# Performance work log

Hardware: AMD Instinct MI355X
Metric: run time of the kernel (lower is better)

Reference implementation:

```python
import jax, jax.numpy as jnp
import numpy as np

NUM_EXPERTS = 64


def setup_inputs() -> dict:
    key = jax.random.key(0)
    k1, k2 = jax.random.split(key)
    x = jax.random.normal(k1, (8192, 4096), dtype=jnp.float32)
    W = jax.random.normal(k2, (NUM_EXPERTS, 4096), dtype=jnp.float32) * 0.02
    return {"x": x, "W": W}


def reference(x, W):
    # gate: logits = x @ W^T  -> [T, E]
    logits = jnp.einsum('th,eh->te', x, W)
    scores = jax.nn.softmax(logits, axis=-1)
    # top_k == 1 path: max with keepdim (torch scores.max(dim=-1, keepdim=True))
    expert_weights = jnp.max(scores, axis=-1, keepdims=True)      # [T, 1]
    expert_indices = jnp.argmax(scores, axis=-1, keepdims=True)   # [T, 1] int
    # routing_counts = bincount(expert_indices.squeeze(1), minlength=E)
    routing_counts = jnp.bincount(expert_indices[:, 0], length=NUM_EXPERTS)
    return (expert_weights, expert_indices, scores, routing_counts)
```

## Files before the change

### kernel.cpp

```cpp
#include <hip/hip_runtime.h>
#include <stdint.h>

#define T_TOKENS 8192
#define K_DIM    4096
#define NEXP     64
#define TB       128
#define KC       64

typedef short bf16x8 __attribute__((ext_vector_type(8)));
typedef float f32x4  __attribute__((ext_vector_type(4)));

__device__ __forceinline__ uint32_t f2bf(float v) {
    uint32_t u = __builtin_bit_cast(uint32_t, v);
    return (u + 0x7fffu + ((u >> 16) & 1u)) >> 16;
}
__device__ __forceinline__ float bf2f(uint32_t b) {
    return __builtin_bit_cast(float, b << 16);
}
struct S3 { short h, l, q; };
__device__ __forceinline__ S3 cvt1(float v) {
    uint32_t hb = f2bf(v); float r  = v - bf2f(hb);
    uint32_t lb = f2bf(r); float r2 = r - bf2f(lb);
    uint32_t qb = f2bf(r2);
    S3 o; o.h = (short)hb; o.l = (short)lb; o.q = (short)qb; return o;
}
__device__ __forceinline__ void cvt8(const float4 a0, const float4 a1,
                                     bf16x8& xh, bf16x8& xl, bf16x8& xq) {
    const float av[8] = {a0.x, a0.y, a0.z, a0.w, a1.x, a1.y, a1.z, a1.w};
#pragma unroll
    for (int j = 0; j < 8; ++j) {
        S3 o = cvt1(av[j]);
        xh[j] = o.h; xl[j] = o.l; xq[j] = o.q;
    }
}

__global__ void wpack(const float* __restrict__ W, float4* __restrict__ Wf,
                      float* __restrict__ out_counts) {
    const int l     = threadIdx.x;
    const int kstep = blockIdx.x;
    const int etile = blockIdx.y;
    if (kstep == 0 && etile == 0)
        out_counts[l] = 0.f;
    const int e = etile * 16 + (l & 15);
    const int k = kstep * 32 + (l >> 4) * 8;
    const float* src = W + (size_t)e * K_DIM + k;
    bf16x8 h, l1, l2;
#pragma unroll
    for (int j = 0; j < 8; ++j) {
        S3 o = cvt1(src[j]);
        h[j] = o.h; l1[j] = o.l; l2[j] = o.q;
    }
    const size_t base = ((size_t)(kstep * 4 + etile) * 3) * 64 + l;
    Wf[base]       = __builtin_bit_cast(float4, h);
    Wf[base + 64]  = __builtin_bit_cast(float4, l1);
    Wf[base + 128] = __builtin_bit_cast(float4, l2);
}

__global__ __launch_bounds__(512, 4) void gemm_mfma(
    const float*  __restrict__ x,
    const float4* __restrict__ Wf,
    float* __restrict__ P,
    int KS)
{
    __shared__ float4 bbuf[2][1536];

    const int tid  = threadIdx.x;
    const int l    = tid & 63;
    const int wv   = __builtin_amdgcn_readfirstlane(tid >> 6);
    const int t0   = blockIdx.x * TB;
    const int slice = blockIdx.y;
    const int k0   = slice * KS;
    const int nchunk = KS / KC;

    const float4* x4 = (const float4*)x;
    const int arow = wv * 16 + (l & 15);
    const size_t xg = (size_t)(t0 + arow) * (K_DIM / 4) + (size_t)(k0 >> 2) + ((l >> 4) * 2);

    const size_t bg0 = ((size_t)(k0 >> 5)) * 768;

    f32x4 acc[4];
#pragma unroll
    for (int et = 0; et < 4; ++et) acc[et] = (f32x4){0.f, 0.f, 0.f, 0.f};

#pragma unroll
    for (int q = 0; q < 3; ++q)
        __builtin_amdgcn_global_load_lds(
            (const __attribute__((address_space(1))) void*)(Wf + bg0 + (wv * 3 + q) * 64 + l),
            (__attribute__((address_space(3))) void*)&bbuf[0][(wv * 3 + q) * 64],
            16, 0, 0);
    float4 xa0 = x4[xg + 0], xa1 = x4[xg + 1];
    float4 xa2 = x4[xg + 8], xa3 = x4[xg + 9];
    asm volatile("s_waitcnt vmcnt(0)" ::: "memory");
    __syncthreads();

    for (int c = 0; c < nchunk; ++c) {
        const int b  = c & 1;
        const int nb = b ^ 1;

        float4 xn0 = xa0, xn1 = xa1, xn2 = xa2, xn3 = xa3;
        if (c + 1 < nchunk) {
            const size_t bo = bg0 + (size_t)(c + 1) * 1536;
#pragma unroll
            for (int q = 0; q < 3; ++q)
                __builtin_amdgcn_global_load_lds(
                    (const __attribute__((address_space(1))) void*)(Wf + bo + (wv * 3 + q) * 64 + l),
                    (__attribute__((address_space(3))) void*)&bbuf[nb][(wv * 3 + q) * 64],
                    16, 0, 0);
            const size_t xo = xg + (size_t)(c + 1) * 16;
            xn0 = x4[xo + 0]; xn1 = x4[xo + 1];
            xn2 = x4[xo + 8]; xn3 = x4[xo + 9];
        }

        bf16x8 xh0, xl0, xq0, xh1, xl1, xq1;
        cvt8(xa0, xa1, xh0, xl0, xq0);
        cvt8(xa2, xa3, xh1, xl1, xq1);

#pragma unroll
        for (int et = 0; et < 4; ++et) {
            {
                const float4* bp = &bbuf[b][et * 192 + l];
                bf16x8 wh = __builtin_bit_cast(bf16x8, bp[0]);
                bf16x8 wl = __builtin_bit_cast(bf16x8, bp[64]);
                bf16x8 wq = __builtin_bit_cast(bf16x8, bp[128]);
                acc[et] = __builtin_amdgcn_mfma_f32_16x16x32_bf16(xh0, wh, acc[et], 0, 0, 0);
                acc[et] = __builtin_amdgcn_mfma_f32_16x16x32_bf16(xh0, wl, acc[et], 0, 0, 0);
                acc[et] = __builtin_amdgcn_mfma_f32_16x16x32_bf16(xh0, wq, acc[et], 0, 0, 0);
                acc[et] = __builtin_amdgcn_mfma_f32_16x16x32_bf16(xl0, wh, acc[et], 0, 0, 0);
                acc[et] = __builtin_amdgcn_mfma_f32_16x16x32_bf16(xl0, wl, acc[et], 0, 0, 0);
                acc[et] = __builtin_amdgcn_mfma_f32_16x16x32_bf16(xq0, wh, acc[et], 0, 0, 0);
            }
            {
                const float4* bp = &bbuf[b][768 + et * 192 + l];
                bf16x8 wh = __builtin_bit_cast(bf16x8, bp[0]);
                bf16x8 wl = __builtin_bit_cast(bf16x8, bp[64]);
                bf16x8 wq = __builtin_bit_cast(bf16x8, bp[128]);
                acc[et] = __builtin_amdgcn_mfma_f32_16x16x32_bf16(xh1, wh, acc[et], 0, 0, 0);
                acc[et] = __builtin_amdgcn_mfma_f32_16x16x32_bf16(xh1, wl, acc[et], 0, 0, 0);
                acc[et] = __builtin_amdgcn_mfma_f32_16x16x32_bf16(xh1, wq, acc[et], 0, 0, 0);
                acc[et] = __builtin_amdgcn_mfma_f32_16x16x32_bf16(xl1, wh, acc[et], 0, 0, 0);
                acc[et] = __builtin_amdgcn_mfma_f32_16x16x32_bf16(xl1, wl, acc[et], 0, 0, 0);
                acc[et] = __builtin_amdgcn_mfma_f32_16x16x32_bf16(xq1, wh, acc[et], 0, 0, 0);
            }
        }

        asm volatile("s_waitcnt vmcnt(0)" ::: "memory");
        __syncthreads();
        xa0 = xn0; xa1 = xn1; xa2 = xn2; xa3 = xn3;
    }

    float* Pp = P + (size_t)slice * T_TOKENS * NEXP;
#pragma unroll
    for (int et = 0; et < 4; ++et) {
#pragma unroll
        for (int i = 0; i < 4; ++i) {
            int t = t0 + wv * 16 + (l >> 4) * 4 + i;
            Pp[(size_t)t * NEXP + et * 16 + (l & 15)] = acc[et][i];
        }
    }
}

template <int S>
__global__ __launch_bounds__(256) void router_finish_t(
    const float* __restrict__ P, float* __restrict__ out)
{
    const int lane = threadIdx.x & 63;
    const int wv   = threadIdx.x >> 6;
    const int t    = blockIdx.x * 4 + wv;

    float lg = 0.f;
#pragma unroll
    for (int s = 0; s < S; ++s)
        lg += P[((size_t)s * T_TOKENS + t) * NEXP + lane];

    float* out_w = out;
    float* out_i = out + T_TOKENS;
    float* out_s = out + 2 * T_TOKENS;
    float* out_c = out + 2 * T_TOKENS + (size_t)T_TOKENS * NEXP;

    float m = lg;
#pragma unroll
    for (int off = 32; off > 0; off >>= 1)
        m = fmaxf(m, __shfl_xor(m, off));
    float p = expf(lg - m);
    float s = p;
#pragma unroll
    for (int off = 32; off > 0; off >>= 1)
        s += __shfl_xor(s, off);
    float sc = p / s;

    float bv = sc; int bi = lane;
#pragma unroll
    for (int off = 32; off > 0; off >>= 1) {
        float ov = __shfl_xor(bv, off);
        int   oi = __shfl_xor(bi, off);
        if (ov > bv || (ov == bv && oi < bi)) { bv = ov; bi = oi; }
    }
    out_s[(size_t)t * NEXP + lane] = sc;
    if (lane == 0) {
        out_w[t] = bv;
        out_i[t] = (float)bi;
        atomicAdd(&out_c[bi], 1.0f);
    }
}

extern "C" void kernel_launch(void* const* d_in, const int* in_sizes, int n_in,
                              void* d_out, int out_size, void* d_ws, size_t ws_size,
                              hipStream_t stream)
{
    const float* x = (const float*)d_in[0];
    const float* W = (const float*)d_in[1];
    float* out = (float*)d_out;
    float* out_s = out + 2 * T_TOKENS;
    float* out_c = out + 2 * T_TOKENS + (size_t)T_TOKENS * NEXP;

    const size_t wf_bytes  = (size_t)128 * 4 * 3 * 64 * 16;
    const size_t per_slice = (size_t)T_TOKENS * NEXP * sizeof(float);

    int S = 8;
    while (S > 1 && wf_bytes + (size_t)S * per_slice > ws_size) S >>= 1;
    float4* Wf = (float4*)d_ws;
    float* Pbuf;
    if (wf_bytes + per_slice <= ws_size) {
        Pbuf = (float*)((char*)d_ws + wf_bytes);
    } else {
        S = 1;
        Pbuf = out_s;
    }

    wpack<<<dim3(128, 4), 64, 0, stream>>>(W, Wf, out_c);
    gemm_mfma<<<dim3(T_TOKENS / TB, S), 512, 0, stream>>>(x, Wf, Pbuf, K_DIM / S);
    switch (S) {
        case 8: router_finish_t<8><<<T_TOKENS / 4, 256, 0, stream>>>(Pbuf, out); break;
        case 4: router_finish_t<4><<<T_TOKENS / 4, 256, 0, stream>>>(Pbuf, out); break;
        case 2: router_finish_t<2><<<T_TOKENS / 4, 256, 0, stream>>>(Pbuf, out); break;
        default: router_finish_t<1><<<T_TOKENS / 4, 256, 0, stream>>>(Pbuf, out); break;
    }
}
```

Baseline: 93.63 us.

## Replace LDS-staged GEMM with register-pipelined 2x2 wave tiling and direct weight loads

```diff
diff --git a/kernel.cpp b/kernel.cpp
--- a/kernel.cpp
+++ b/kernel.cpp
@@ -5,7 +5,6 @@
 #define K_DIM    4096
 #define NEXP     64
 #define TB       128
-#define KC       64
 
 typedef short bf16x8 __attribute__((ext_vector_type(8)));
 typedef float f32x4  __attribute__((ext_vector_type(4)));
@@ -56,105 +55,90 @@
     Wf[base + 128] = __builtin_bit_cast(float4, l2);
 }
 
-__global__ __launch_bounds__(512, 4) void gemm_mfma(
+template <int NCH>
+__global__ __launch_bounds__(512, 2) void gemm_mfma(
     const float*  __restrict__ x,
     const float4* __restrict__ Wf,
-    float* __restrict__ P,
-    int KS)
+    float* __restrict__ P)
 {
-    __shared__ float4 bbuf[2][1536];
-
     const int tid  = threadIdx.x;
     const int l    = tid & 63;
     const int wv   = __builtin_amdgcn_readfirstlane(tid >> 6);
-    const int t0   = blockIdx.x * TB;
-    const int slice = blockIdx.y;
-    const int k0   = slice * KS;
-    const int nchunk = KS / KC;
+    const int rg   = wv >> 1;
+    const int cg   = wv & 1;
+    const int slice = blockIdx.x;
+    const int t0    = blockIdx.y * TB;
+    const int k0    = slice * (NCH * 32);
 
     const float4* x4 = (const float4*)x;
-    const int arow = wv * 16 + (l & 15);
-    const size_t xg = (size_t)(t0 + arow) * (K_DIM / 4) + (size_t)(k0 >> 2) + ((l >> 4) * 2);
-
-    const size_t bg0 = ((size_t)(k0 >> 5)) * 768;
-
-    f32x4 acc[4];
-#pragma unroll
-    for (int et = 0; et < 4; ++et) acc[et] = (f32x4){0.f, 0.f, 0.f, 0.f};
-
-#pragma unroll
-    for (int q = 0; q < 3; ++q)
-        __builtin_amdgcn_global_load_lds(
-            (const __attribute__((address_space(1))) void*)(Wf + bg0 + (wv * 3 + q) * 64 + l),
-            (__attribute__((address_space(3))) void*)&bbuf[0][(wv * 3 + q) * 64],
-            16, 0, 0);
-    float4 xa0 = x4[xg + 0], xa1 = x4[xg + 1];
-    float4 xa2 = x4[xg + 8], xa3 = x4[xg + 9];
-    asm volatile("s_waitcnt vmcnt(0)" ::: "memory");
-    __syncthreads();
-
-    for (int c = 0; c < nchunk; ++c) {
-        const int b  = c & 1;
-        const int nb = b ^ 1;
-
-        float4 xn0 = xa0, xn1 = xa1, xn2 = xa2, xn3 = xa3;
-        if (c + 1 < nchunk) {
-            const size_t bo = bg0 + (size_t)(c + 1) * 1536;
-#pragma unroll
-            for (int q = 0; q < 3; ++q)
-                __builtin_amdgcn_global_load_lds(
-                    (const __attribute__((address_space(1))) void*)(Wf + bo + (wv * 3 + q) * 64 + l),
-                    (__attribute__((address_space(3))) void*)&bbuf[nb][(wv * 3 + q) * 64],
-                    16, 0, 0);
-            const size_t xo = xg + (size_t)(c + 1) * 16;
-            xn0 = x4[xo + 0]; xn1 = x4[xo + 1];
-            xn2 = x4[xo + 8]; xn3 = x4[xo + 9];
+    const size_t xr0 = (size_t)(t0 + rg * 32 + (l & 15)) * (K_DIM / 4)
+                     + (size_t)(k0 >> 2) + ((l >> 4) * 2);
+    const size_t xr1 = xr0 + (size_t)16 * (K_DIM / 4);
+    const float4* bb = Wf + (((size_t)(k0 >> 5) * 4 + cg * 2) * 3) * 64 + l;
+
+    f32x4 acc00 = {0,0,0,0}, acc01 = {0,0,0,0};
+    f32x4 acc10 = {0,0,0,0}, acc11 = {0,0,0,0};
+
+    float4 xs[3][4];
+    float4 bs[3][6];
+
+#define LOADK(ks, slot)                                                        \
+    do {                                                                       \
+        const size_t xo = (size_t)(ks) * 8;                                    \
+        xs[slot][0] = x4[xr0 + xo];     xs[slot][1] = x4[xr0 + xo + 1];        \
+        xs[slot][2] = x4[xr1 + xo];     xs[slot][3] = x4[xr1 + xo + 1];        \
+        const float4* bp = bb + (size_t)(ks) * 768;                            \
+        bs[slot][0] = bp[0];   bs[slot][1] = bp[64];  bs[slot][2] = bp[128];   \
+        bs[slot][3] = bp[192]; bs[slot][4] = bp[256]; bs[slot][5] = bp[320];   \
+    } while (0)
+
+    LOADK(0, 0);
+    LOADK(1, 1);
+
+#pragma unroll
+    for (int ks = 0; ks < NCH; ++ks) {
+        if (ks + 2 < NCH) LOADK(ks + 2, (ks + 2) % 3);
+        const int s = ks % 3;
+
+        bf16x8 xh0, xl0, xq0, xh1, xl1, xq1;
+        cvt8(xs[s][0], xs[s][1], xh0, xl0, xq0);
+        cvt8(xs[s][2], xs[s][3], xh1, xl1, xq1);
+
+#pragma unroll
+        for (int e = 0; e < 2; ++e) {
+            bf16x8 wh = __builtin_bit_cast(bf16x8, bs[s][e * 3 + 0]);
+            bf16x8 wl = __builtin_bit_cast(bf16x8, bs[s][e * 3 + 1]);
+            bf16x8 wq = __builtin_bit_cast(bf16x8, bs[s][e * 3 + 2]);
+            f32x4& a0 = e ? acc10 : acc00;
+            f32x4& a1 = e ? acc11 : acc01;
+            a0 = __builtin_amdgcn_mfma_f32_16x16x32_bf16(xh0, wh, a0, 0, 0, 0);
+            a0 = __builtin_amdgcn_mfma_f32_16x16x32_bf16(xh0, wl, a0, 0, 0, 0);
+            a0 = __builtin_amdgcn_mfma_f32_16x16x32_bf16(xh0, wq, a0, 0, 0, 0);
+            a0 = __builtin_amdgcn_mfma_f32_16x16x32_bf16(xl0, wh, a0, 0, 0, 0);
+            a0 = __builtin_amdgcn_mfma_f32_16x16x32_bf16(xl0, wl, a0, 0, 0, 0);
+            a0 = __builtin_amdgcn_mfma_f32_16x16x32_bf16(xq0, wh, a0, 0, 0, 0);
+            a1 = __builtin_amdgcn_mfma_f32_16x16x32_bf16(xh1, wh, a1, 0, 0, 0);
+            a1 = __builtin_amdgcn_mfma_f32_16x16x32_bf16(xh1, wl, a1, 0, 0, 0);
+            a1 = __builtin_amdgcn_mfma_f32_16x16x32_bf16(xh1, wq, a1, 0, 0, 0);
+            a1 = __builtin_amdgcn_mfma_f32_16x16x32_bf16(xl1, wh, a1, 0, 0, 0);
+            a1 = __builtin_amdgcn_mfma_f32_16x16x32_bf16(xl1, wl, a1, 0, 0, 0);
+            a1 = __builtin_amdgcn_mfma_f32_16x16x32_bf16(xq1, wh, a1, 0, 0, 0);
         }
-
-        bf16x8 xh0, xl0, xq0, xh1, xl1, xq1;
-        cvt8(xa0, xa1, xh0, xl0, xq0);
-        cvt8(xa2, xa3, xh1, xl1, xq1);
-
-#pragma unroll
-        for (int et = 0; et < 4; ++et) {
-            {
-                const float4* bp = &bbuf[b][et * 192 + l];
-                bf16x8 wh = __builtin_bit_cast(bf16x8, bp[0]);
-                bf16x8 wl = __builtin_bit_cast(bf16x8, bp[64]);
-                bf16x8 wq = __builtin_bit_cast(bf16x8, bp[128]);
-                acc[et] = __builtin_amdgcn_mfma_f32_16x16x32_bf16(xh0, wh, acc[et], 0, 0, 0);
-                acc[et] = __builtin_amdgcn_mfma_f32_16x16x32_bf16(xh0, wl, acc[et], 0, 0, 0);
-                acc[et] = __builtin_amdgcn_mfma_f32_16x16x32_bf16(xh0, wq, acc[et], 0, 0, 0);
-                acc[et] = __builtin_amdgcn_mfma_f32_16x16x32_bf16(xl0, wh, acc[et], 0, 0, 0);
-                acc[et] = __builtin_amdgcn_mfma_f32_16x16x32_bf16(xl0, wl, acc[et], 0, 0, 0);
-                acc[et] = __builtin_amdgcn_mfma_f32_16x16x32_bf16(xq0, wh, acc[et], 0, 0, 0);
+    }
+#undef LOADK
+
+    float* Pp = P + (size_t)slice * T_TOKENS * NEXP;
+#pragma unroll
+    for (int e = 0; e < 2; ++e) {
+#pragma unroll
+        for (int rt = 0; rt < 2; ++rt) {
+            const f32x4 a = e ? (rt ? acc11 : acc10) : (rt ? acc01 : acc00);
+            const int ecol = (cg * 2 + e) * 16 + (l & 15);
+#pragma unroll
+            for (int i = 0; i < 4; ++i) {
+                int t = t0 + rg * 32 + rt * 16 + (l >> 4) * 4 + i;
+                Pp[(size_t)t * NEXP + ecol] = a[i];
             }
-            {
-                const float4* bp = &bbuf[b][768 + et * 192 + l];
-                bf16x8 wh = __builtin_bit_cast(bf16x8, bp[0]);
-                bf16x8 wl = __builtin_bit_cast(bf16x8, bp[64]);
-                bf16x8 wq = __builtin_bit_cast(bf16x8, bp[128]);
-                acc[et] = __builtin_amdgcn_mfma_f32_16x16x32_bf16(xh1, wh, acc[et], 0, 0, 0);
-                acc[et] = __builtin_amdgcn_mfma_f32_16x16x32_bf16(xh1, wl, acc[et], 0, 0, 0);
-                acc[et] = __builtin_amdgcn_mfma_f32_16x16x32_bf16(xh1, wq, acc[et], 0, 0, 0);
-                acc[et] = __builtin_amdgcn_mfma_f32_16x16x32_bf16(xl1, wh, acc[et], 0, 0, 0);
-                acc[et] = __builtin_amdgcn_mfma_f32_16x16x32_bf16(xl1, wl, acc[et], 0, 0, 0);
-                acc[et] = __builtin_amdgcn_mfma_f32_16x16x32_bf16(xq1, wh, acc[et], 0, 0, 0);
-            }
-        }
-
-        asm volatile("s_waitcnt vmcnt(0)" ::: "memory");
-        __syncthreads();
-        xa0 = xn0; xa1 = xn1; xa2 = xn2; xa3 = xn3;
-    }
-
-    float* Pp = P + (size_t)slice * T_TOKENS * NEXP;
-#pragma unroll
-    for (int et = 0; et < 4; ++et) {
-#pragma unroll
-        for (int i = 0; i < 4; ++i) {
-            int t = t0 + wv * 16 + (l >> 4) * 4 + i;
-            Pp[(size_t)t * NEXP + et * 16 + (l & 15)] = acc[et][i];
         }
     }
 }
@@ -228,7 +212,12 @@
     }
 
     wpack<<<dim3(128, 4), 64, 0, stream>>>(W, Wf, out_c);
-    gemm_mfma<<<dim3(T_TOKENS / TB, S), 512, 0, stream>>>(x, Wf, Pbuf, K_DIM / S);
+    switch (S) {
+        case 8: gemm_mfma<16> <<<dim3(8, T_TOKENS / TB), 512, 0, stream>>>(x, Wf, Pbuf); break;
+        case 4: gemm_mfma<32> <<<dim3(4, T_TOKENS / TB), 512, 0, stream>>>(x, Wf, Pbuf); break;
+        case 2: gemm_mfma<64> <<<dim3(2, T_TOKENS / TB), 512, 0, stream>>>(x, Wf, Pbuf); break;
+        default: gemm_mfma<128><<<dim3(1, T_TOKENS / TB), 512, 0, stream>>>(x, Wf, Pbuf); break;
+    }
     switch (S) {
         case 8: router_finish_t<8><<<T_TOKENS / 4, 256, 0, stream>>>(Pbuf, out); break;
         case 4: router_finish_t<4><<<T_TOKENS / 4, 256, 0, stream>>>(Pbuf, out); break;
```

Measured after the change: 110.4 us. 1.18x slower.
